# Kernel optimization log

Hardware: AMD Instinct MI355X
Metric: run time of the kernel (lower is better)

The kernel has to match this reference:

```python
import math
import jax, jax.numpy as jnp
import numpy as np

HIDDEN = 1280
N_HEADS = 10
HEAD_DIM = HIDDEN // N_HEADS  # 128
ROPE_BASE = 10000.0
EPS = 1e-5


def _rope_freqs(head_dim, base):
    half = head_dim // 2
    return -jnp.exp(jnp.arange(0.0, half, dtype=jnp.float32) * (math.log(base) / half))


def apply_rotary_emb(x, offset=0, freqs=None):
    # x: (B, H, T, D), blocked (non-interleaved) RoPE layout
    B, H, T, D = x.shape
    if freqs is None:
        freqs = _rope_freqs(D, ROPE_BASE)
    positions = jnp.arange(offset, offset + T, dtype=jnp.float32)
    angles = jnp.outer(positions, freqs)          # (T, D/2)
    cos = jnp.cos(angles)
    sin = jnp.sin(angles)
    x1 = x[..., : D // 2]
    x2 = x[..., D // 2 :]
    rx1 = x1 * cos - x2 * sin
    rx2 = x2 * cos + x1 * sin
    return jnp.concatenate([rx1, rx2], axis=-1)


def rms_norm(x):
    return x * jax.lax.rsqrt(jnp.mean(jnp.square(x), axis=-1, keepdims=True) + EPS)


def setup_inputs() -> dict:
    key = jax.random.key(0)
    ks = jax.random.split(key, 5)
    B, L = 4, 2048
    s = 1.0 / math.sqrt(HIDDEN)
    return {
        "x": jax.random.normal(ks[0], (B, L, HIDDEN), dtype=jnp.float32),
        "wq": jax.random.normal(ks[1], (HIDDEN, HIDDEN), dtype=jnp.float32) * s,
        "wk": jax.random.normal(ks[2], (HIDDEN, HIDDEN), dtype=jnp.float32) * s,
        "wv": jax.random.normal(ks[3], (HIDDEN, HIDDEN), dtype=jnp.float32) * s,
        "wo": jax.random.normal(ks[4], (HIDDEN, HIDDEN), dtype=jnp.float32) * s,
    }


def reference(x, wq, wk, wv, wo):
    B, L, _ = x.shape
    scale = HEAD_DIM ** -0.5
    # QKV projections (Linear with weight W: y = x @ W.T)
    q = (x @ wq.T).reshape(B, L, N_HEADS, HEAD_DIM).transpose(0, 2, 1, 3)  # (B,H,L,D)
    k = (x @ wk.T).reshape(B, L, N_HEADS, HEAD_DIM).transpose(0, 2, 1, 3)
    v = (x @ wv.T).reshape(B, L, N_HEADS, HEAD_DIM).transpose(0, 2, 1, 3)
    freqs = _rope_freqs(HEAD_DIM, ROPE_BASE)
    q = rms_norm(apply_rotary_emb(q, 0, freqs))
    k = rms_norm(apply_rotary_emb(k, 0, freqs))
    # SDPA (no mask, matching mask=None path)
    scores = jnp.einsum("bhqd,bhkd->bhqk", q, k) * scale
    attn = jax.nn.softmax(scores, axis=-1)
    out = jnp.einsum("bhqk,bhkd->bhqd", attn, v)
    out = out.transpose(0, 2, 1, 3).reshape(B, L, HIDDEN)
    return out @ wo.T
```

## Files before the change

### kernel.cpp

```cpp
#include <hip/hip_runtime.h>
#include <math.h>

typedef unsigned short u16;
typedef unsigned long long u64;
typedef __attribute__((ext_vector_type(8))) short bf16x8;
typedef __attribute__((ext_vector_type(4))) float f32x4;
typedef __attribute__((ext_vector_type(4))) unsigned short u16x4;

#define MFMA16(a,b,c) __builtin_amdgcn_mfma_f32_16x16x32_bf16((a),(b),(c),0,0,0)

static constexpr int kHid = 1280;
static constexpr int kSeq = 2048;
static constexpr int kNH  = 10;
static constexpr int kHD  = 128;
static constexpr int kB   = 4;
static constexpr int kBL  = kB * kSeq;

__device__ __forceinline__ u16 f2bf(float f) {
  union { float f; unsigned u; } a; a.f = f;
  unsigned r = a.u + 0x7fffu + ((a.u >> 16) & 1u);
  return (u16)(r >> 16);
}
__device__ __forceinline__ float bf2f(u16 h) {
  union { unsigned u; float f; } a; a.u = ((unsigned)h) << 16;
  return a.f;
}

__device__ __forceinline__ void gll16(const void* g, void* l) {
  __builtin_amdgcn_global_load_lds((__attribute__((address_space(1))) void*)(g),
                                   (__attribute__((address_space(3))) void*)(l), 16, 0, 0);
}

__global__ __launch_bounds__(256) void cvt_bf16(const float* __restrict__ s,
                                                u16* __restrict__ d, int n4) {
  int i = blockIdx.x * 256 + threadIdx.x;
  if (i >= n4) return;
  float4 v = ((const float4*)s)[i];
  u16x4 o;
  o.x = f2bf(v.x); o.y = f2bf(v.y); o.z = f2bf(v.z); o.w = f2bf(v.w);
  ((u16x4*)d)[i] = o;
}

__global__ __launch_bounds__(256) void cvt_split(const float* __restrict__ s,
                                                 u16* __restrict__ dh,
                                                 u16* __restrict__ dl, int n4) {
  int i = blockIdx.x * 256 + threadIdx.x;
  if (i >= n4) return;
  float4 v = ((const float4*)s)[i];
  u16x4 oh, ol;
  oh.x = f2bf(v.x); ol.x = f2bf(v.x - bf2f(oh.x));
  oh.y = f2bf(v.y); ol.y = f2bf(v.y - bf2f(oh.y));
  oh.z = f2bf(v.z); ol.z = f2bf(v.z - bf2f(oh.z));
  oh.w = f2bf(v.w); ol.w = f2bf(v.w - bf2f(oh.w));
  ((u16x4*)dh)[i] = oh;
  ((u16x4*)dl)[i] = ol;
}

__device__ __forceinline__ double frac_of(int d, float* rout) {
  const float C = (float)(9.210340371976184 / 64.0);
  float a = (float)d * C;
  double e = exp((double)a);
  float r = (float)e;
  double fr;
  if (e >= (double)r) {
    float up = __int_as_float(__float_as_int(r) + 1);
    fr = (e - (double)r) / ((double)up - (double)r);
  } else {
    float dn = __int_as_float(__float_as_int(r) - 1);
    fr = (e - (double)r) / ((double)r - (double)dn);
  }
  *rout = r;
  return fr;
}

__global__ __launch_bounds__(256) void rope_tab(float* __restrict__ ct, float* __restrict__ st) {
  int i = blockIdx.x * 256 + threadIdx.x;
  if (i >= kSeq * 64) return;
  int t = i >> 6, d = i & 63;

  int dF = -1; double bm = 0.40; float rF = 1.0f;
  for (int dd = 38; dd <= 58; dd++) {
    float rr; double fr = frac_of(dd, &rr);
    if (fabs(fr) > bm) { bm = fabs(fr); dF = dd; rF = rr; }
  }
  const int binF = (dF >= 0) ? ilogbf(rF) : -9999;

  float r; double fr = frac_of(d, &r);
  double w = 0.0;
  if (d != dF && ilogbf(r) == binF) {
    double af = fabs(fr);
    w = (af >= 0.03 && af <= 0.32) ? 0.472 : 0.35;
  }
  int dir = (fr >= 0.0) ? 1 : -1;
  float rB = __int_as_float(__float_as_int(r) + dir);

  float A  = (float)t * (-r);
  float A2 = (float)t * (-rB);
  float c  = cosf(A),  s  = sinf(A);
  float c2 = cosf(A2), s2 = sinf(A2);
  float wf = (float)w;
  ct[i] = c + wf * (c2 - c);
  st[i] = s + wf * (s2 - s);
}

__global__ __launch_bounds__(256) void gemm_qkv(
    const u16* __restrict__ Ah, const u16* __restrict__ Al,
    const u16* __restrict__ Wh, const u16* __restrict__ Wl,
    const float* __restrict__ ct, const float* __restrict__ st,
    u16* __restrict__ qh, u16* __restrict__ ql,
    u16* __restrict__ kh, u16* __restrict__ kl,
    u16* __restrict__ vt)
{
  __shared__ u16 Bsh[128 * 32];
  __shared__ u16 Bsl[128 * 32];
  const int bn = blockIdx.x;
  if (bn >= 30) return;
  const int tid = threadIdx.x;
  const int w = tid >> 6, lane = tid & 63;
  const int c15 = lane & 15, q8 = lane >> 4;
  const int m0 = blockIdx.y * 128;
  const int n0 = bn * 128;
  const bool split = (bn < 20);

  const f32x4 vzero = {0.f, 0.f, 0.f, 0.f};
  f32x4 acc[2][8];
#pragma unroll
  for (int i = 0; i < 2; i++)
#pragma unroll
    for (int j = 0; j < 8; j++) acc[i][j] = vzero;

  const int sr = w * 32 + (lane >> 2);
  const int sc = lane & 3;
  const size_t ra0 = (size_t)(m0 + w * 32 + c15) * kHid + q8 * 8;
  const size_t ra1 = (size_t)(m0 + w * 32 + 16 + c15) * kHid + q8 * 8;

  for (int k0 = 0; k0 < kHid; k0 += 32) {
    bf16x8 a0h, a1h, a0l, a1l;
    a0h = *(const bf16x8*)&Ah[ra0 + k0];
    a1h = *(const bf16x8*)&Ah[ra1 + k0];
    if (split) {
      a0l = *(const bf16x8*)&Al[ra0 + k0];
      a1l = *(const bf16x8*)&Al[ra1 + k0];
    }
#pragma unroll
    for (int i = 0; i < 2; i++) {
      int r = sr + i * 16;
      int gc = (sc ^ ((r >> 1) & 3)) << 3;
      size_t gb = (size_t)(n0 + r) * kHid + k0 + gc;
      gll16(Wh + gb, &Bsh[(w * 32 + i * 16) * 32]);
      if (split) gll16(Wl + gb, &Bsl[(w * 32 + i * 16) * 32]);
    }
    __syncthreads();
#pragma unroll
    for (int ni = 0; ni < 8; ni++) {
      int rb = ni * 16 + c15;
      int ob = rb * 32 + ((q8 ^ ((rb >> 1) & 3)) << 3);
      bf16x8 bbh = *(const bf16x8*)&Bsh[ob];
      acc[0][ni] = MFMA16(a0h, bbh, acc[0][ni]);
      acc[1][ni] = MFMA16(a1h, bbh, acc[1][ni]);
      if (split) {
        bf16x8 bbl = *(const bf16x8*)&Bsl[ob];
        acc[0][ni] = MFMA16(a0h, bbl, acc[0][ni]);
        acc[1][ni] = MFMA16(a1h, bbl, acc[1][ni]);
        acc[0][ni] = MFMA16(a0l, bbh, acc[0][ni]);
        acc[1][ni] = MFMA16(a1l, bbh, acc[1][ni]);
      }
    }
    __syncthreads();
  }

  const int typ = bn / 10, h = bn % 10;
#pragma unroll
  for (int mi = 0; mi < 2; mi++) {
#pragma unroll
    for (int rg = 0; rg < 4; rg++) {
      int n = m0 + w * 32 + mi * 16 + q8 * 4 + rg;
      int b = n >> 11, t = n & 2047;
      if (typ == 2) {
        size_t base = ((size_t)(b * kNH + h) * kHD) * kSeq + t;
#pragma unroll
        for (int ni = 0; ni < 8; ni++) {
          int d = ni * 16 + c15;
          vt[base + (size_t)d * kSeq] = f2bf(acc[mi][ni][rg]);
        }
      } else {
        float rv[8]; float ss = 0.f;
#pragma unroll
        for (int ni = 0; ni < 4; ni++) {
          int d = ni * 16 + c15;
          float cs = ct[t * 64 + d], sn = st[t * 64 + d];
          float x1 = acc[mi][ni][rg], x2 = acc[mi][ni + 4][rg];
          float r1 = x1 * cs - x2 * sn;
          float r2 = x2 * cs + x1 * sn;
          rv[ni] = r1; rv[ni + 4] = r2;
          ss += r1 * r1 + r2 * r2;
        }
#pragma unroll
        for (int off = 1; off < 16; off <<= 1) ss += __shfl_xor(ss, off, 64);
        float sc2 = rsqrtf(ss * (1.f / 128.f) + 1e-5f);
        u16* dsth = (typ == 0) ? qh : kh;
        u16* dstl = (typ == 0) ? ql : kl;
        size_t base = ((size_t)(b * kNH + h) * kSeq + t) * kHD;
#pragma unroll
        for (int ni = 0; ni < 8; ni++) {
          float val = rv[ni] * sc2;
          u16 hi = f2bf(val);
          dsth[base + ni * 16 + c15] = hi;
          dstl[base + ni * 16 + c15] = f2bf(val - bf2f(hi));
        }
      }
    }
  }
}

__global__ __launch_bounds__(256, 2) void attn_fwd(
    const u16* __restrict__ qhp, const u16* __restrict__ qlp,
    const u16* __restrict__ khp, const u16* __restrict__ klp,
    const u16* __restrict__ vt, u16* __restrict__ ao)
{
  __shared__ __align__(16) u16 smem[3 * 64 * 128];
  u16* const Ksh = smem;
  u16* const Ksl = smem + 64 * 128;
  u16* const Vs  = smem + 2 * 64 * 128;
  u16* const Ps  = smem;
  const int tid = threadIdx.x;
  const int w = tid >> 6, lane = tid & 63;
  const int c15 = lane & 15, q8 = lane >> 4;
  const int qt = blockIdx.x;
  const int bh = blockIdx.y;
  const int b = bh / kNH, h = bh % kNH;
  const size_t kvbase = (size_t)bh * kSeq * kHD;
  const int qr0 = qt * 128 + w * 32;

  bf16x8 qfh[4][2], qfl[4][2];
#pragma unroll
  for (int kd = 0; kd < 4; kd++)
#pragma unroll
    for (int mi = 0; mi < 2; mi++) {
      size_t off = kvbase + (size_t)(qr0 + mi * 16 + c15) * kHD + kd * 32 + q8 * 8;
      qfh[kd][mi] = *(const bf16x8*)&qhp[off];
      qfl[kd][mi] = *(const bf16x8*)&qlp[off];
    }

  const f32x4 vzero = {0.f, 0.f, 0.f, 0.f};
  f32x4 oacc[2][8];
#pragma unroll
  for (int i = 0; i < 2; i++)
#pragma unroll
    for (int j = 0; j < 8; j++) oacc[i][j] = vzero;
  float ms[2][4], ls[2][4];
#pragma unroll
  for (int i = 0; i < 2; i++)
#pragma unroll
    for (int j = 0; j < 4; j++) { ms[i][j] = -3.0e38f; ls[i][j] = 0.f; }

  const float SL2E = 0.08838834764831845f * 1.4426950408889634f;

  for (int kt = 0; kt < kSeq / 64; kt++) {
    const int kv0 = kt * 64;
#pragma unroll
    for (int i = 0; i < 4; i++) {
      int r = w * 16 + i * 4 + (lane >> 4);
      size_t g = kvbase + (size_t)(kv0 + r) * kHD + (((lane & 15) ^ (r & 7)) << 3);
      gll16(khp + g, &Ksh[(w * 16 + i * 4) * 128]);
      gll16(klp + g, &Ksl[(w * 16 + i * 4) * 128]);
    }
#pragma unroll
    for (int i = 0; i < 4; i++) {
      int d = w * 32 + i * 8 + (lane >> 3);
      gll16(vt + kvbase + (size_t)d * kSeq + kv0 + (((lane & 7) ^ (d & 7)) << 3),
            &Vs[(w * 32 + i * 8) * 64]);
    }
    __syncthreads();

    f32x4 sacc[2][4];
#pragma unroll
    for (int i = 0; i < 2; i++)
#pragma unroll
      for (int j = 0; j < 4; j++) sacc[i][j] = vzero;
    __builtin_amdgcn_s_setprio(1);
#pragma unroll
    for (int kd = 0; kd < 4; kd++) {
#pragma unroll
      for (int nk = 0; nk < 4; nk++) {
        int rb = nk * 16 + c15;
        int ob = rb * 128 + ((((kd << 2) + q8) ^ (rb & 7)) << 3);
        bf16x8 kbh = *(const bf16x8*)&Ksh[ob];
        bf16x8 kbl = *(const bf16x8*)&Ksl[ob];
        sacc[0][nk] = MFMA16(qfh[kd][0], kbh, sacc[0][nk]);
        sacc[0][nk] = MFMA16(qfh[kd][0], kbl, sacc[0][nk]);
        sacc[0][nk] = MFMA16(qfl[kd][0], kbh, sacc[0][nk]);
        sacc[1][nk] = MFMA16(qfh[kd][1], kbh, sacc[1][nk]);
        sacc[1][nk] = MFMA16(qfh[kd][1], kbl, sacc[1][nk]);
        sacc[1][nk] = MFMA16(qfl[kd][1], kbh, sacc[1][nk]);
      }
    }
    __builtin_amdgcn_s_setprio(0);
    __syncthreads();

#pragma unroll
    for (int mi = 0; mi < 2; mi++) {
#pragma unroll
      for (int rg = 0; rg < 4; rg++) {
        float v0 = sacc[mi][0][rg] * SL2E;
        float v1 = sacc[mi][1][rg] * SL2E;
        float v2 = sacc[mi][2][rg] * SL2E;
        float v3 = sacc[mi][3][rg] * SL2E;
        float mt = fmaxf(fmaxf(v0, v1), fmaxf(v2, v3));
#pragma unroll
        for (int off = 1; off < 16; off <<= 1) mt = fmaxf(mt, __shfl_xor(mt, off, 64));
        float mold = ms[mi][rg];
        float mnew = fmaxf(mold, mt);
        float alpha = exp2f(mold - mnew);
        float p0 = exp2f(v0 - mnew), p1 = exp2f(v1 - mnew);
        float p2 = exp2f(v2 - mnew), p3 = exp2f(v3 - mnew);
        float psum = (p0 + p1) + (p2 + p3);
#pragma unroll
        for (int off = 1; off < 16; off <<= 1) psum += __shfl_xor(psum, off, 64);
        ls[mi][rg] = ls[mi][rg] * alpha + psum;
        ms[mi][rg] = mnew;
#pragma unroll
        for (int nd = 0; nd < 8; nd++) oacc[mi][nd][rg] = oacc[mi][nd][rg] * alpha;
        int pr = w * 32 + mi * 16 + q8 * 4 + rg;
        Ps[pr * 72 +      c15] = f2bf(p0);
        Ps[pr * 72 + 16 + c15] = f2bf(p1);
        Ps[pr * 72 + 32 + c15] = f2bf(p2);
        Ps[pr * 72 + 48 + c15] = f2bf(p3);
      }
    }

    __builtin_amdgcn_s_setprio(1);
#pragma unroll
    for (int kk = 0; kk < 2; kk++) {
      bf16x8 pa0 = *(const bf16x8*)&Ps[(w * 32 + c15) * 72 + kk * 32 + q8 * 8];
      bf16x8 pa1 = *(const bf16x8*)&Ps[(w * 32 + 16 + c15) * 72 + kk * 32 + q8 * 8];
#pragma unroll
      for (int nd = 0; nd < 8; nd++) {
        int d = nd * 16 + c15;
        bf16x8 vb = *(const bf16x8*)&Vs[d * 64 + ((((kk << 2) + q8) ^ (d & 7)) << 3)];
        oacc[0][nd] = MFMA16(pa0, vb, oacc[0][nd]);
        oacc[1][nd] = MFMA16(pa1, vb, oacc[1][nd]);
      }
    }
    __builtin_amdgcn_s_setprio(0);
    __syncthreads();
  }

#pragma unroll
  for (int mi = 0; mi < 2; mi++) {
#pragma unroll
    for (int rg = 0; rg < 4; rg++) {
      int t = qr0 + mi * 16 + q8 * 4 + rg;
      float inv = 1.0f / ls[mi][rg];
      size_t base = ((size_t)(b * kSeq + t)) * kHid + h * kHD;
#pragma unroll
      for (int nd = 0; nd < 8; nd++)
        ao[base + nd * 16 + c15] = f2bf(oacc[mi][nd][rg] * inv);
    }
  }
}

__global__ __launch_bounds__(256) void gemm_out(
    const u16* __restrict__ A, const u16* __restrict__ Bw, float* __restrict__ out)
{
  __shared__ u16 As[128 * 32];
  __shared__ u16 Bs[128 * 32];
  const int tid = threadIdx.x;
  const int w = tid >> 6, lane = tid & 63;
  const int c15 = lane & 15, q8 = lane >> 4;
  const int m0 = blockIdx.y * 128;
  const int n0 = blockIdx.x * 128;

  const f32x4 vzero = {0.f, 0.f, 0.f, 0.f};
  f32x4 acc[2][8];
#pragma unroll
  for (int i = 0; i < 2; i++)
#pragma unroll
    for (int j = 0; j < 8; j++) acc[i][j] = vzero;

  const int sr = w * 32 + (lane >> 2);
  const int sc = lane & 3;

  for (int k0 = 0; k0 < kHid; k0 += 32) {
#pragma unroll
    for (int i = 0; i < 2; i++) {
      int r = sr + i * 16;
      int gc = (sc ^ ((r >> 1) & 3)) << 3;
      gll16(A  + (size_t)(m0 + r) * kHid + k0 + gc, &As[(w * 32 + i * 16) * 32]);
      gll16(Bw + (size_t)(n0 + r) * kHid + k0 + gc, &Bs[(w * 32 + i * 16) * 32]);
    }
    __syncthreads();
    bf16x8 a0, a1;
    { int r = w * 32 + c15;      a0 = *(const bf16x8*)&As[r * 32 + ((q8 ^ ((r >> 1) & 3)) << 3)]; }
    { int r = w * 32 + 16 + c15; a1 = *(const bf16x8*)&As[r * 32 + ((q8 ^ ((r >> 1) & 3)) << 3)]; }
#pragma unroll
    for (int ni = 0; ni < 8; ni++) {
      int rb = ni * 16 + c15;
      bf16x8 bb = *(const bf16x8*)&Bs[rb * 32 + ((q8 ^ ((rb >> 1) & 3)) << 3)];
      acc[0][ni] = MFMA16(a0, bb, acc[0][ni]);
      acc[1][ni] = MFMA16(a1, bb, acc[1][ni]);
    }
    __syncthreads();
  }

#pragma unroll
  for (int mi = 0; mi < 2; mi++) {
#pragma unroll
    for (int rg = 0; rg < 4; rg++) {
      int n = m0 + w * 32 + mi * 16 + q8 * 4 + rg;
      float* orow = out + (size_t)n * kHid + n0;
#pragma unroll
      for (int ni = 0; ni < 8; ni++) orow[ni * 16 + c15] = acc[mi][ni][rg];
    }
  }
}

extern "C" void kernel_launch(void* const* d_in, const int* in_sizes, int n_in,
                              void* d_out, int out_size, void* d_ws, size_t ws_size,
                              hipStream_t stream) {
  (void)in_sizes; (void)n_in; (void)out_size; (void)ws_size;
  const float* x  = (const float*)d_in[0];
  const float* wq = (const float*)d_in[1];
  const float* wk = (const float*)d_in[2];
  const float* wv = (const float*)d_in[3];
  const float* wo = (const float*)d_in[4];
  float* out = (float*)d_out;

  u16* xh    = (u16*)d_ws;
  u16* xl    = xh    + (size_t)kBL * kHid;
  u16* wqkvh = xl    + (size_t)kBL * kHid;
  u16* wqkl  = wqkvh + (size_t)3 * kHid * kHid;
  u16* woh   = wqkl  + (size_t)2 * kHid * kHid;
  u16* qhb   = woh   + (size_t)kHid * kHid;
  u16* qlb   = qhb   + (size_t)kB * kNH * kSeq * kHD;
  u16* khb   = qlb   + (size_t)kB * kNH * kSeq * kHD;
  u16* klb   = khb   + (size_t)kB * kNH * kSeq * kHD;
  u16* vtb   = klb   + (size_t)kB * kNH * kSeq * kHD;
  u16* aob   = vtb   + (size_t)kB * kNH * kSeq * kHD;
  float* ct  = (float*)(aob + (size_t)kBL * kHid);
  float* st  = ct + (size_t)kSeq * 64;

  const int n4x = kBL * kHid / 4;
  const int n4w = kHid * kHid / 4;
  cvt_split<<<(n4x + 255) / 256, 256, 0, stream>>>(x, xh, xl, n4x);
  cvt_split<<<(n4w + 255) / 256, 256, 0, stream>>>(wq, wqkvh, wqkl, n4w);
  cvt_split<<<(n4w + 255) / 256, 256, 0, stream>>>(wk, wqkvh + (size_t)kHid * kHid,
                                                  wqkl + (size_t)kHid * kHid, n4w);
  cvt_bf16<<<(n4w + 255) / 256, 256, 0, stream>>>(wv, wqkvh + (size_t)2 * kHid * kHid, n4w);
  cvt_bf16<<<(n4w + 255) / 256, 256, 0, stream>>>(wo, woh, n4w);
  rope_tab<<<(kSeq * 64 + 255) / 256, 256, 0, stream>>>(ct, st);

  gemm_qkv<<<dim3(32, 64), 256, 0, stream>>>(xh, xl, wqkvh, wqkl, ct, st,
                                             qhb, qlb, khb, klb, vtb);
  attn_fwd<<<dim3(16, 40), 256, 0, stream>>>(qhb, qlb, khb, klb, vtb, aob);
  gemm_out<<<dim3(10, 64), 256, 0, stream>>>(aob, woh, out);
}
```

Before: 812.2 us.

## Fuse weight conversions, add lazy softmax rescale, pad out-proj grid

The four weight-conversion launches become a single cvt_weights kernel. In attention, the online-softmax rescale of the accumulator and row sum now runs only when some lane's new row max exceeds the old one by more than 8 (log2 units). Otherwise the old max stays in place, which removes the exp2 and the 16 multiplies on most iterations but lets unnormalised probabilities grow up to 256x. The output GEMM grid is enlarged to 16 columns, and blocks with x at 10 or above exit at once, so those blocks only add launch overhead.

```diff
diff --git a/kernel.cpp b/kernel.cpp
--- a/kernel.cpp
+++ b/kernel.cpp
@@ -29,16 +29,6 @@
 __device__ __forceinline__ void gll16(const void* g, void* l) {
   __builtin_amdgcn_global_load_lds((__attribute__((address_space(1))) void*)(g),
                                    (__attribute__((address_space(3))) void*)(l), 16, 0, 0);
-}
-
-__global__ __launch_bounds__(256) void cvt_bf16(const float* __restrict__ s,
-                                                u16* __restrict__ d, int n4) {
-  int i = blockIdx.x * 256 + threadIdx.x;
-  if (i >= n4) return;
-  float4 v = ((const float4*)s)[i];
-  u16x4 o;
-  o.x = f2bf(v.x); o.y = f2bf(v.y); o.z = f2bf(v.z); o.w = f2bf(v.w);
-  ((u16x4*)d)[i] = o;
 }
 
 __global__ __launch_bounds__(256) void cvt_split(const float* __restrict__ s,
@@ -54,6 +44,33 @@
   oh.w = f2bf(v.w); ol.w = f2bf(v.w - bf2f(oh.w));
   ((u16x4*)dh)[i] = oh;
   ((u16x4*)dl)[i] = ol;
+}
+
+__global__ __launch_bounds__(256) void cvt_weights(
+    const float* __restrict__ wq, const float* __restrict__ wk,
+    const float* __restrict__ wv, const float* __restrict__ wo,
+    u16* __restrict__ wqkvh, u16* __restrict__ wqkl,
+    u16* __restrict__ woh, int n4w) {
+  int i = blockIdx.x * 256 + threadIdx.x;
+  int sel = i / n4w;
+  int j = i - sel * n4w;
+  if (sel >= 4) return;
+  const float* src = (sel == 0) ? wq : (sel == 1) ? wk : (sel == 2) ? wv : wo;
+  float4 v = ((const float4*)src)[j];
+  if (sel < 2) {
+    u16x4 oh, ol;
+    oh.x = f2bf(v.x); ol.x = f2bf(v.x - bf2f(oh.x));
+    oh.y = f2bf(v.y); ol.y = f2bf(v.y - bf2f(oh.y));
+    oh.z = f2bf(v.z); ol.z = f2bf(v.z - bf2f(oh.z));
+    oh.w = f2bf(v.w); ol.w = f2bf(v.w - bf2f(oh.w));
+    ((u16x4*)wqkvh)[(size_t)sel * n4w + j] = oh;
+    ((u16x4*)wqkl)[(size_t)sel * n4w + j]  = ol;
+  } else {
+    u16x4 o;
+    o.x = f2bf(v.x); o.y = f2bf(v.y); o.z = f2bf(v.z); o.w = f2bf(v.w);
+    if (sel == 2) ((u16x4*)wqkvh)[(size_t)2 * n4w + j] = o;
+    else          ((u16x4*)woh)[j] = o;
+  }
 }
 
 __device__ __forceinline__ double frac_of(int d, float* rout) {
@@ -310,17 +327,22 @@
 #pragma unroll
         for (int off = 1; off < 16; off <<= 1) mt = fmaxf(mt, __shfl_xor(mt, off, 64));
         float mold = ms[mi][rg];
-        float mnew = fmaxf(mold, mt);
-        float alpha = exp2f(mold - mnew);
+        bool nskip = !__all(mt - mold <= 8.0f);
+        float mnew = nskip ? fmaxf(mold, mt) : mold;
         float p0 = exp2f(v0 - mnew), p1 = exp2f(v1 - mnew);
         float p2 = exp2f(v2 - mnew), p3 = exp2f(v3 - mnew);
         float psum = (p0 + p1) + (p2 + p3);
 #pragma unroll
         for (int off = 1; off < 16; off <<= 1) psum += __shfl_xor(psum, off, 64);
-        ls[mi][rg] = ls[mi][rg] * alpha + psum;
-        ms[mi][rg] = mnew;
-#pragma unroll
-        for (int nd = 0; nd < 8; nd++) oacc[mi][nd][rg] = oacc[mi][nd][rg] * alpha;
+        if (nskip) {
+          float alpha = exp2f(mold - mnew);
+          ls[mi][rg] = ls[mi][rg] * alpha + psum;
+          ms[mi][rg] = mnew;
+#pragma unroll
+          for (int nd = 0; nd < 8; nd++) oacc[mi][nd][rg] = oacc[mi][nd][rg] * alpha;
+        } else {
+          ls[mi][rg] += psum;
+        }
         int pr = w * 32 + mi * 16 + q8 * 4 + rg;
         Ps[pr * 72 +      c15] = f2bf(p0);
         Ps[pr * 72 + 16 + c15] = f2bf(p1);
@@ -365,11 +387,13 @@
 {
   __shared__ u16 As[128 * 32];
   __shared__ u16 Bs[128 * 32];
+  const int bx = blockIdx.x;
+  if (bx >= 10) return;
   const int tid = threadIdx.x;
   const int w = tid >> 6, lane = tid & 63;
   const int c15 = lane & 15, q8 = lane >> 4;
   const int m0 = blockIdx.y * 128;
-  const int n0 = blockIdx.x * 128;
+  const int n0 = bx * 128;
 
   const f32x4 vzero = {0.f, 0.f, 0.f, 0.f};
   f32x4 acc[2][8];
@@ -443,15 +467,12 @@
   const int n4x = kBL * kHid / 4;
   const int n4w = kHid * kHid / 4;
   cvt_split<<<(n4x + 255) / 256, 256, 0, stream>>>(x, xh, xl, n4x);
-  cvt_split<<<(n4w + 255) / 256, 256, 0, stream>>>(wq, wqkvh, wqkl, n4w);
-  cvt_split<<<(n4w + 255) / 256, 256, 0, stream>>>(wk, wqkvh + (size_t)kHid * kHid,
-                                                  wqkl + (size_t)kHid * kHid, n4w);
-  cvt_bf16<<<(n4w + 255) / 256, 256, 0, stream>>>(wv, wqkvh + (size_t)2 * kHid * kHid, n4w);
-  cvt_bf16<<<(n4w + 255) / 256, 256, 0, stream>>>(wo, woh, n4w);
+  cvt_weights<<<(4 * n4w) / 256, 256, 0, stream>>>(wq, wk, wv, wo,
+                                                   wqkvh, wqkl, woh, n4w);
   rope_tab<<<(kSeq * 64 + 255) / 256, 256, 0, stream>>>(ct, st);
 
   gemm_qkv<<<dim3(32, 64), 256, 0, stream>>>(xh, xl, wqkvh, wqkl, ct, st,
                                              qhb, qlb, khb, klb, vtb);
   attn_fwd<<<dim3(16, 40), 256, 0, stream>>>(qhb, qlb, khb, klb, vtb, aob);
-  gemm_out<<<dim3(10, 64), 256, 0, stream>>>(aob, woh, out);
-}
+  gemm_out<<<dim3(16, 64), 256, 0, stream>>>(aob, woh, out);
+}
```

After: 868.8 us. 1.07x slower.
